# Kernel tuning notes

Measured on AMD Instinct MI355X. Metric: run time of the kernel, lower is better.

## Reference

```python
import jax, jax.numpy as jnp
import numpy as np

T, B, I, H = 512, 64, 256, 256
ACT_EXP2 = 7   # activation scale = 2^-7
W_EXP2 = 8     # weight scale = 2^-8
QMIN, QMAX = -128.0, 127.0  # int8 symmetric, zp=0


def fq(x, exp2_inv):
    """Fake-quantize (round/clamp/dequant) with straight-through estimator."""
    scale = 2.0 ** (-exp2_inv)
    y = jnp.clip(jnp.round(x / scale), QMIN, QMAX) * scale
    return x + jax.lax.stop_gradient(y - x)


def setup_inputs() -> dict:
    key = jax.random.key(0)
    k = jax.random.split(key, 5)
    x = jax.random.normal(k[0], (T, B, I), jnp.float32)
    h0 = jnp.zeros((B, H), jnp.float32)
    W = jax.random.normal(k[1], (I, 3 * H), jnp.float32) / np.sqrt(I)
    R = jax.random.normal(k[2], (H, 3 * H), jnp.float32) / np.sqrt(H)
    bx = jax.random.normal(k[3], (3 * H,), jnp.float32) * 0.1
    br = jax.random.normal(k[4], (3 * H,), jnp.float32) * 0.1
    return {"x": x, "h0": h0, "W": W, "R": R, "bx": bx, "br": br}


def gru_quant(x, h0, W, R, bx, br):
    # quantize weights/biases once (weight.W / weight.R / weight.bx / weight.br)
    Wq = fq(W, W_EXP2)
    Rq = fq(R, W_EXP2)
    bxq = fq(bx, W_EXP2)
    brq = fq(br, W_EXP2)
    # hoisted input matmul: Wx = fq(fq(x) @ Wq)  -> [T, B, 3H]
    Wx = fq(jnp.einsum('tbi,ij->tbj', fq(x, ACT_EXP2), Wq), ACT_EXP2)
    Hh = h0.shape[-1]
    bz, brg, bg = bxq[:Hh], bxq[Hh:2 * Hh], bxq[2 * Hh:]

    def step(h, wx_t):
        hq = fq(h, ACT_EXP2)                      # input.h
        Rh = fq(hq @ Rq, ACT_EXP2)                # matmul.Rh
        v = fq(Rh + brq, ACT_EXP2)                # op.Rh_add_br
        wz, wr, wg = wx_t[:, :Hh], wx_t[:, Hh:2 * Hh], wx_t[:, 2 * Hh:]
        vz, vr, vg = v[:, :Hh], v[:, Hh:2 * Hh], v[:, 2 * Hh:]
        z = fq(jax.nn.sigmoid(fq(wz + bz + vz, ACT_EXP2)), ACT_EXP2)  # gate.z
        r = fq(jax.nn.sigmoid(fq(wr + brg + vr, ACT_EXP2)), ACT_EXP2)  # gate.r
        rRh = fq(r * vg, ACT_EXP2)                # op.rRh
        g = fq(jnp.tanh(fq(wg + bg + rRh, ACT_EXP2)), ACT_EXP2)        # gate.g
        old = fq(z * h, ACT_EXP2)                 # op.old_contrib
        new = fq((1.0 - z) * g, ACT_EXP2)         # op.new_contrib
        h_new = old + new
        return h_new, h_new

    _, hs = jax.lax.scan(step, h0, Wx)  # hs: [T, B, H]
    return hs


def reference(x, h0, W, R, bx, br):
    return gru_quant(x, h0, W, R, bx, br)
```

## Files before the change

kernel.cpp:

```cpp
#include <hip/hip_runtime.h>
#include <hip/hip_bf16.h>
#include <stdint.h>


#define T_STEPS 512
#define BATCH   64
#define IDIM    256
#define HDIM    256
#define N3H     768

#if defined(__has_builtin)
#if __has_builtin(__builtin_amdgcn_sdot4)
#define DOT4(a,b,c) __builtin_amdgcn_sdot4((int)(a),(int)(b),(int)(c),false)
#endif
#endif
#ifndef DOT4
__device__ __forceinline__ int dot4_sw(uint32_t a, uint32_t b, int c){
  c += (int)(int8_t)(a)      * (int)(int8_t)(b);
  c += (int)(int8_t)(a>>8)   * (int)(int8_t)(b>>8);
  c += (int)(int8_t)(a>>16)  * (int)(int8_t)(b>>16);
  c += (int)(int8_t)(a>>24)  * (int)(int8_t)(b>>24);
  return c;
}
#define DOT4(a,b,c) dot4_sw((uint32_t)(a),(uint32_t)(b),(int)(c))
#endif

#define CHUNK(W,c) (((c)&3)==0 ? W[(c)>>2].x : ((c)&3)==1 ? W[(c)>>2].y : \
                    ((c)&3)==2 ? W[(c)>>2].z : W[(c)>>2].w)

__device__ __forceinline__ void barrier_lds() {
  asm volatile("s_waitcnt lgkmcnt(0)\n\ts_barrier" ::: "memory");
}

__device__ __forceinline__ int clamp8(int x)   { return min(127, max(-128, x)); }
__device__ __forceinline__ int rne_half(int y) { int t = y >> 1; return t + (t & y & 1); }
__device__ __forceinline__ int rne_s8(int s)   { return (s + 127 + ((s >> 8) & 1)) >> 8; }
__device__ __forceinline__ int rne_s7(int p)   { return (p + 63 + ((p >> 7) & 1)) >> 7; }

__device__ __forceinline__ int rneclamp(float v) {
  int q = (int)rintf(v);
  return min(127, max(-128, q));
}

__device__ __forceinline__ uint32_t packq4(float4 f, float sc) {
  uint32_t b0 = (uint32_t)(uint8_t)(int8_t)rneclamp(f.x * sc);
  uint32_t b1 = (uint32_t)(uint8_t)(int8_t)rneclamp(f.y * sc);
  uint32_t b2 = (uint32_t)(uint8_t)(int8_t)rneclamp(f.z * sc);
  uint32_t b3 = (uint32_t)(uint8_t)(int8_t)rneclamp(f.w * sc);
  return b0 | (b1 << 8) | (b2 << 16) | (b3 << 24);
}

__global__ void prep_kernel(const float* __restrict__ W, const float* __restrict__ R,
                            const float* __restrict__ bx, const float* __restrict__ br,
                            int8_t* __restrict__ Wq, int8_t* __restrict__ Rq,
                            int8_t* __restrict__ bx8, int8_t* __restrict__ br8) {
  const int NW = IDIM * N3H;
  int idx = blockIdx.x * 256 + threadIdx.x;
  if (idx < NW) {
    int k = idx / N3H, j = idx % N3H;
    Wq[((size_t)(k >> 4) * N3H + j) * 16 + (k & 15)] = (int8_t)rneclamp(W[idx] * 256.0f);
  } else if (idx < 2 * NW) {
    int i2 = idx - NW;
    int k = i2 / N3H, j = i2 % N3H;
    Rq[(size_t)j * HDIM + k] = (int8_t)rneclamp(R[i2] * 256.0f);
  } else if (idx < 2 * NW + N3H) {
    int i2 = idx - 2 * NW;
    bx8[i2] = (int8_t)rneclamp(bx[i2] * 256.0f);
  } else if (idx < 2 * NW + 2 * N3H) {
    int i2 = idx - 2 * NW - N3H;
    br8[i2] = (int8_t)rneclamp(br[i2] * 256.0f);
  }
}

__global__ __launch_bounds__(768, 1) void gemm_wx_kernel(
    const float* __restrict__ x, const int8_t* __restrict__ Wq,
    int8_t* __restrict__ WxQ8) {
  const int t = blockIdx.x;
  const int j = threadIdx.x;

  __shared__ uint4 xq4[64 * 16];
  uint32_t* xq = (uint32_t*)xq4;

  uint4 w[16];
  const uint4* wp = (const uint4*)Wq;
  #pragma unroll
  for (int kk = 0; kk < 16; ++kk) w[kk] = wp[kk * N3H + j];

  const float4* xg = (const float4*)(x) + (size_t)t * 4096;
  for (int i = j; i < 4096; i += 768) {
    float4 f = xg[i];
    xq[i] = packq4(f, 128.0f);
  }
  __syncthreads();

  for (int r = 0; r < 64; ++r) {
    int s = 0;
    #pragma unroll
    for (int kk = 0; kk < 16; ++kk) {
      uint4 hv = xq4[r * 16 + kk];
      s = DOT4(hv.x, w[kk].x, s);
      s = DOT4(hv.y, w[kk].y, s);
      s = DOT4(hv.z, w[kk].z, s);
      s = DOT4(hv.w, w[kk].w, s);
    }
    int q = clamp8(rne_s8(s));
    WxQ8[((size_t)r * T_STEPS + t) * N3H + j] = (int8_t)q;
  }
}

__global__ __launch_bounds__(256, 1) __attribute__((amdgpu_waves_per_eu(1, 1)))
void gru_rec6_kernel(
    const float* __restrict__ h0, const int8_t* __restrict__ Rq,
    const int8_t* __restrict__ bx8, const int8_t* __restrict__ br8,
    const int8_t* __restrict__ WxQ8, float* __restrict__ out) {
  const int b = blockIdx.x;
  const int j = threadIdx.x;
  const int lane = j & 63;

  __shared__ uint32_t hq[2][64];
  __shared__ int8_t lutS[256];
  __shared__ int8_t lutT[256];

  uint4 wz[16], wr[16], wg[16];
  {
    const uint4* pz = (const uint4*)(Rq + (size_t)j * HDIM);
    const uint4* pr = (const uint4*)(Rq + (size_t)(j + 256) * HDIM);
    const uint4* pg = (const uint4*)(Rq + (size_t)(j + 512) * HDIM);
    #pragma unroll
    for (int kk = 0; kk < 16; ++kk) { wz[kk] = pz[kk]; wr[kk] = pr[kk]; wg[kk] = pg[kk]; }
  }
  const int bz  = (int)bx8[j];
  const int brg = (int)bx8[j + 256];
  const int bg  = (int)bx8[j + 512];
  const int vbz = (int)br8[j];
  const int vbr = (int)br8[j + 256];
  const int vbg = (int)br8[j + 512];

  {
    double a = ((double)j - 128.0) / 128.0;
    lutS[j] = (int8_t)min(127, max(-128, (int)rint(128.0 / (1.0 + exp(-a)))));
    lutT[j] = (int8_t)min(127, max(-128, (int)rint(128.0 * tanh(a))));
  }
  int hi = (int)rintf(h0[b * HDIM + j] * 128.0f);
  ((int8_t*)&hq[0][0])[j] = (int8_t)clamp8(hi);
  __syncthreads();

  const int8_t* wxp = WxQ8 + (size_t)b * T_STEPS * N3H + j;
  float* outp = out + (size_t)b * HDIM + j;

  int wxA0 = (int)wxp[0],   wxA1 = (int)wxp[256],       wxA2 = (int)wxp[512];
  int wxB0 = (int)wxp[N3H], wxB1 = (int)wxp[N3H + 256], wxB2 = (int)wxp[N3H + 512];

  for (int t = 0; t < T_STEPS; ++t) {
    const int cur = t & 1, nxt = cur ^ 1;

    const int8_t* p = wxp + (size_t)min(t + 2, T_STEPS - 1) * N3H;
    int nz = (int)p[0], nr = (int)p[256], ng = (int)p[512];

    uint32_t hw = hq[cur][lane];
    int sz = 0, sr = 0, sg = 0;
    #pragma unroll
    for (int c = 0; c < 64; ++c) {
      int hc = __builtin_amdgcn_readlane((int)hw, c);
      sz = DOT4(hc, CHUNK(wz, c), sz);
      sr = DOT4(hc, CHUNK(wr, c), sr);
      sg = DOT4(hc, CHUNK(wg, c), sg);
    }
    int vz = clamp8(rne_half(2 * clamp8(rne_s8(sz)) + vbz));
    int vr = clamp8(rne_half(2 * clamp8(rne_s8(sr)) + vbr));
    int vg = clamp8(rne_half(2 * clamp8(rne_s8(sg)) + vbg));

    int az = clamp8(rne_half(2 * (wxA0 + vz) + bz));
    int zi = (int)lutS[az + 128];
    int ar = clamp8(rne_half(2 * (wxA1 + vr) + brg));
    int ri = (int)lutS[ar + 128];
    int rrh = clamp8(rne_s7(ri * vg));
    int ag = clamp8(rne_half(2 * (wxA2 + rrh) + bg));
    int gi = (int)lutT[ag + 128];
    int oldi = clamp8(rne_s7(zi * hi));
    int newi = clamp8(rne_s7((128 - zi) * gi));
    hi = oldi + newi;
    outp[(size_t)t * BATCH * HDIM] = (float)hi * (1.0f / 128.0f);
    ((int8_t*)&hq[nxt][0])[j] = (int8_t)clamp8(hi);

    wxA0 = wxB0; wxA1 = wxB1; wxA2 = wxB2;
    wxB0 = nz;   wxB1 = nr;   wxB2 = ng;

    barrier_lds();
  }
}

extern "C" void kernel_launch(void* const* d_in, const int* in_sizes, int n_in,
                              void* d_out, int out_size, void* d_ws, size_t ws_size,
                              hipStream_t stream) {
  const float* x  = (const float*)d_in[0];
  const float* h0 = (const float*)d_in[1];
  const float* W  = (const float*)d_in[2];
  const float* R  = (const float*)d_in[3];
  const float* bx = (const float*)d_in[4];
  const float* br = (const float*)d_in[5];
  float* out = (float*)d_out;

  const size_t NW = (size_t)IDIM * N3H;
  int8_t* Wq  = (int8_t*)d_ws;
  int8_t* Rq  = Wq + NW;
  int8_t* bx8 = Rq + NW;
  int8_t* br8 = bx8 + N3H;
  int8_t* WxQ8 = br8 + N3H;

  {
    int total = (int)(2 * NW + 2 * N3H);
    int blocks = (total + 255) / 256;
    prep_kernel<<<blocks, 256, 0, stream>>>(W, R, bx, br, Wq, Rq, bx8, br8);
  }
  gemm_wx_kernel<<<T_STEPS, 768, 0, stream>>>(x, Wq, WxQ8);
  gru_rec6_kernel<<<BATCH, 256, 0, stream>>>(h0, Rq, bx8, br8, WxQ8, out);
}
```

Baseline: 473.9 us.

## Split recurrent matvec across 768 threads, one gate column per thread

The recurrent kernel now launches 768 threads per batch block instead of 256. Each thread computes one of the 3H gate outputs, holding a single 256-byte weight column in registers rather than three, and the R weights are stored in the same k-chunked layout as W. Gate pre-activations go through a shared-memory buffer plus an extra barrier per step, and the first 256 threads then do the elementwise GRU update. This spreads the serial per-step dot-product work over three times as many waves, at the cost of a second barrier each step and idle threads during the elementwise phase.

```diff
diff --git a/kernel.cpp b/kernel.cpp
--- a/kernel.cpp
+++ b/kernel.cpp
@@ -62,7 +62,7 @@
   } else if (idx < 2 * NW) {
     int i2 = idx - NW;
     int k = i2 / N3H, j = i2 % N3H;
-    Rq[(size_t)j * HDIM + k] = (int8_t)rneclamp(R[i2] * 256.0f);
+    Rq[((size_t)(k >> 4) * N3H + j) * 16 + (k & 15)] = (int8_t)rneclamp(R[i2] * 256.0f);
   } else if (idx < 2 * NW + N3H) {
     int i2 = idx - 2 * NW;
     bx8[i2] = (int8_t)rneclamp(bx[i2] * 256.0f);
@@ -108,8 +108,8 @@
   }
 }
 
-__global__ __launch_bounds__(256, 1) __attribute__((amdgpu_waves_per_eu(1, 1)))
-void gru_rec6_kernel(
+__global__ __launch_bounds__(768, 3)
+void gru_rec13_kernel(
     const float* __restrict__ h0, const int8_t* __restrict__ Rq,
     const int8_t* __restrict__ bx8, const int8_t* __restrict__ br8,
     const int8_t* __restrict__ WxQ8, float* __restrict__ out) {
@@ -118,74 +118,81 @@
   const int lane = j & 63;
 
   __shared__ uint32_t hq[2][64];
+  __shared__ int8_t vbuf[N3H];
   __shared__ int8_t lutS[256];
   __shared__ int8_t lutT[256];
 
-  uint4 wz[16], wr[16], wg[16];
+  uint4 w[16];
   {
-    const uint4* pz = (const uint4*)(Rq + (size_t)j * HDIM);
-    const uint4* pr = (const uint4*)(Rq + (size_t)(j + 256) * HDIM);
-    const uint4* pg = (const uint4*)(Rq + (size_t)(j + 512) * HDIM);
-    #pragma unroll
-    for (int kk = 0; kk < 16; ++kk) { wz[kk] = pz[kk]; wr[kk] = pr[kk]; wg[kk] = pg[kk]; }
-  }
-  const int bz  = (int)bx8[j];
-  const int brg = (int)bx8[j + 256];
-  const int bg  = (int)bx8[j + 512];
-  const int vbz = (int)br8[j];
-  const int vbr = (int)br8[j + 256];
-  const int vbg = (int)br8[j + 512];
-
-  {
+    const uint4* rp = (const uint4*)Rq;
+    #pragma unroll
+    for (int kk = 0; kk < 16; ++kk) w[kk] = rp[kk * N3H + j];
+  }
+  const int vb = (int)br8[j];
+
+  int hi = 0, bzc = 0, brc = 0, bgc = 0;
+  const int8_t* wxp = WxQ8 + (size_t)b * T_STEPS * N3H + j;
+  int wxA0 = 0, wxA1 = 0, wxA2 = 0, wxB0 = 0, wxB1 = 0, wxB2 = 0;
+  if (j < 256) {
     double a = ((double)j - 128.0) / 128.0;
     lutS[j] = (int8_t)min(127, max(-128, (int)rint(128.0 / (1.0 + exp(-a)))));
     lutT[j] = (int8_t)min(127, max(-128, (int)rint(128.0 * tanh(a))));
-  }
-  int hi = (int)rintf(h0[b * HDIM + j] * 128.0f);
-  ((int8_t*)&hq[0][0])[j] = (int8_t)clamp8(hi);
+    bzc = (int)bx8[j];
+    brc = (int)bx8[j + 256];
+    bgc = (int)bx8[j + 512];
+    hi = (int)rintf(h0[b * HDIM + j] * 128.0f);
+    ((int8_t*)&hq[0][0])[j] = (int8_t)clamp8(hi);
+    wxA0 = (int)wxp[0];   wxA1 = (int)wxp[256];       wxA2 = (int)wxp[512];
+    wxB0 = (int)wxp[N3H]; wxB1 = (int)wxp[N3H + 256]; wxB2 = (int)wxp[N3H + 512];
+  }
   __syncthreads();
 
-  const int8_t* wxp = WxQ8 + (size_t)b * T_STEPS * N3H + j;
-  float* outp = out + (size_t)b * HDIM + j;
-
-  int wxA0 = (int)wxp[0],   wxA1 = (int)wxp[256],       wxA2 = (int)wxp[512];
-  int wxB0 = (int)wxp[N3H], wxB1 = (int)wxp[N3H + 256], wxB2 = (int)wxp[N3H + 512];
+  float* outp = out + (size_t)b * HDIM + (j < 256 ? j : 0);
 
   for (int t = 0; t < T_STEPS; ++t) {
     const int cur = t & 1, nxt = cur ^ 1;
 
-    const int8_t* p = wxp + (size_t)min(t + 2, T_STEPS - 1) * N3H;
-    int nz = (int)p[0], nr = (int)p[256], ng = (int)p[512];
+    #pragma unroll
+    for (int kk = 0; kk < 16; ++kk)
+      asm volatile("" : "+v"(w[kk].x), "+v"(w[kk].y), "+v"(w[kk].z), "+v"(w[kk].w));
+
+    int nz = 0, nr = 0, ng = 0;
+    if (j < 256) {
+      const int8_t* p = wxp + (size_t)min(t + 2, T_STEPS - 1) * N3H;
+      nz = (int)p[0]; nr = (int)p[256]; ng = (int)p[512];
+    }
 
     uint32_t hw = hq[cur][lane];
-    int sz = 0, sr = 0, sg = 0;
-    #pragma unroll
-    for (int c = 0; c < 64; ++c) {
-      int hc = __builtin_amdgcn_readlane((int)hw, c);
-      sz = DOT4(hc, CHUNK(wz, c), sz);
-      sr = DOT4(hc, CHUNK(wr, c), sr);
-      sg = DOT4(hc, CHUNK(wg, c), sg);
-    }
-    int vz = clamp8(rne_half(2 * clamp8(rne_s8(sz)) + vbz));
-    int vr = clamp8(rne_half(2 * clamp8(rne_s8(sr)) + vbr));
-    int vg = clamp8(rne_half(2 * clamp8(rne_s8(sg)) + vbg));
-
-    int az = clamp8(rne_half(2 * (wxA0 + vz) + bz));
-    int zi = (int)lutS[az + 128];
-    int ar = clamp8(rne_half(2 * (wxA1 + vr) + brg));
-    int ri = (int)lutS[ar + 128];
-    int rrh = clamp8(rne_s7(ri * vg));
-    int ag = clamp8(rne_half(2 * (wxA2 + rrh) + bg));
-    int gi = (int)lutT[ag + 128];
-    int oldi = clamp8(rne_s7(zi * hi));
-    int newi = clamp8(rne_s7((128 - zi) * gi));
-    hi = oldi + newi;
-    outp[(size_t)t * BATCH * HDIM] = (float)hi * (1.0f / 128.0f);
-    ((int8_t*)&hq[nxt][0])[j] = (int8_t)clamp8(hi);
-
-    wxA0 = wxB0; wxA1 = wxB1; wxA2 = wxB2;
-    wxB0 = nz;   wxB1 = nr;   wxB2 = ng;
-
+    int s0 = 0, s1 = 0;
+    #pragma unroll
+    for (int c = 0; c < 64; c += 2) {
+      int h0c = __builtin_amdgcn_readlane((int)hw, c);
+      int h1c = __builtin_amdgcn_readlane((int)hw, c + 1);
+      s0 = DOT4(h0c, CHUNK(w, c), s0);
+      s1 = DOT4(h1c, CHUNK(w, c + 1), s1);
+    }
+    int s = s0 + s1;
+    int v = clamp8(rne_half(2 * clamp8(rne_s8(s)) + vb));
+    vbuf[j] = (int8_t)v;
+    barrier_lds();
+
+    if (j < 256) {
+      int vz = (int)vbuf[j], vr = (int)vbuf[j + 256], vg = (int)vbuf[j + 512];
+      int az = clamp8(rne_half(2 * (wxA0 + vz) + bzc));
+      int zi = (int)lutS[az + 128];
+      int ar = clamp8(rne_half(2 * (wxA1 + vr) + brc));
+      int ri = (int)lutS[ar + 128];
+      int rrh = clamp8(rne_s7(ri * vg));
+      int ag = clamp8(rne_half(2 * (wxA2 + rrh) + bgc));
+      int gi = (int)lutT[ag + 128];
+      int oldi = clamp8(rne_s7(zi * hi));
+      int newi = clamp8(rne_s7((128 - zi) * gi));
+      hi = oldi + newi;
+      outp[(size_t)t * BATCH * HDIM] = (float)hi * (1.0f / 128.0f);
+      ((int8_t*)&hq[nxt][0])[j] = (int8_t)clamp8(hi);
+      wxA0 = wxB0; wxA1 = wxB1; wxA2 = wxB2;
+      wxB0 = nz;   wxB1 = nr;   wxB2 = ng;
+    }
     barrier_lds();
   }
 }
@@ -214,5 +221,5 @@
     prep_kernel<<<blocks, 256, 0, stream>>>(W, R, bx, br, Wq, Rq, bx8, br8);
   }
   gemm_wx_kernel<<<T_STEPS, 768, 0, stream>>>(x, Wq, WxQ8);
-  gru_rec6_kernel<<<BATCH, 256, 0, stream>>>(h0, Rq, bx8, br8, WxQ8, out);
-}
+  gru_rec13_kernel<<<BATCH, 768, 0, stream>>>(h0, Rq, bx8, br8, WxQ8, out);
+}
```

Result: slower. 629.0 us (+32.7%).

## Split recurrent K dimension across two thread halves and pair two batches per block

Applied to the files above, without the earlier changes.

The recurrent kernel now runs 512 threads per block, each handling two batch rows. Each half of the block computes half of the K reduction for both batches, swaps partial sums through LDS, and then finishes one batch's gate math. The aim is to halve the serial dot-product chain per timestep and reuse register-resident weights across two batches. In exchange it adds a second barrier per step, extra LDS traffic, and uses only 32 blocks.

```diff
diff --git a/kernel.cpp b/kernel.cpp
--- a/kernel.cpp
+++ b/kernel.cpp
@@ -108,48 +108,57 @@
   }
 }
 
-__global__ __launch_bounds__(256, 1) __attribute__((amdgpu_waves_per_eu(1, 1)))
-void gru_rec6_kernel(
+__global__ __launch_bounds__(512, 1)
+void gru_rec17_kernel(
     const float* __restrict__ h0, const int8_t* __restrict__ Rq,
     const int8_t* __restrict__ bx8, const int8_t* __restrict__ br8,
     const int8_t* __restrict__ WxQ8, float* __restrict__ out) {
-  const int b = blockIdx.x;
-  const int j = threadIdx.x;
-  const int lane = j & 63;
-
-  __shared__ uint32_t hq[2][64];
+  const int bA = blockIdx.x * 2;
+  const int bB = bA + 1;
+  const int tid = threadIdx.x;
+  const int kh  = tid >> 8;
+  const int j   = tid & 255;
+  const int lane = tid & 63;
+
+  __shared__ uint32_t hqA[2][64];
+  __shared__ uint32_t hqB[2][64];
+  __shared__ int pubA[3][256];
+  __shared__ int pubB[3][256];
   __shared__ int8_t lutS[256];
   __shared__ int8_t lutT[256];
 
-  uint4 wz[16], wr[16], wg[16];
+  uint4 wz[8], wr[8], wg[8];
   {
-    const uint4* pz = (const uint4*)(Rq + (size_t)j * HDIM);
-    const uint4* pr = (const uint4*)(Rq + (size_t)(j + 256) * HDIM);
-    const uint4* pg = (const uint4*)(Rq + (size_t)(j + 512) * HDIM);
+    const uint4* pz = (const uint4*)(Rq + (size_t)j * HDIM)         + kh * 8;
+    const uint4* pr = (const uint4*)(Rq + (size_t)(j + 256) * HDIM) + kh * 8;
+    const uint4* pg = (const uint4*)(Rq + (size_t)(j + 512) * HDIM) + kh * 8;
     #pragma unroll
-    for (int kk = 0; kk < 16; ++kk) { wz[kk] = pz[kk]; wr[kk] = pr[kk]; wg[kk] = pg[kk]; }
-  }
-  const int bz  = (int)bx8[j];
-  const int brg = (int)bx8[j + 256];
-  const int bg  = (int)bx8[j + 512];
+    for (int kk = 0; kk < 8; ++kk) { wz[kk] = pz[kk]; wr[kk] = pr[kk]; wg[kk] = pg[kk]; }
+  }
+  const int myb = kh ? bB : bA;
+  const int bzc = (int)bx8[j];
+  const int brc = (int)bx8[j + 256];
+  const int bgc = (int)bx8[j + 512];
   const int vbz = (int)br8[j];
   const int vbr = (int)br8[j + 256];
   const int vbg = (int)br8[j + 512];
 
-  {
+  if (tid < 256) {
     double a = ((double)j - 128.0) / 128.0;
     lutS[j] = (int8_t)min(127, max(-128, (int)rint(128.0 / (1.0 + exp(-a)))));
     lutT[j] = (int8_t)min(127, max(-128, (int)rint(128.0 * tanh(a))));
-  }
-  int hi = (int)rintf(h0[b * HDIM + j] * 128.0f);
-  ((int8_t*)&hq[0][0])[j] = (int8_t)clamp8(hi);
-  __syncthreads();
-
-  const int8_t* wxp = WxQ8 + (size_t)b * T_STEPS * N3H + j;
-  float* outp = out + (size_t)b * HDIM + j;
-
+    int hA0 = (int)rintf(h0[bA * HDIM + j] * 128.0f);
+    int hB0 = (int)rintf(h0[bB * HDIM + j] * 128.0f);
+    ((int8_t*)&hqA[0][0])[j] = (int8_t)clamp8(hA0);
+    ((int8_t*)&hqB[0][0])[j] = (int8_t)clamp8(hB0);
+  }
+  int hi = (int)rintf(h0[myb * HDIM + j] * 128.0f);
+
+  const int8_t* wxp = WxQ8 + (size_t)myb * T_STEPS * N3H + j;
+  float* outp = out + (size_t)myb * HDIM + j;
   int wxA0 = (int)wxp[0],   wxA1 = (int)wxp[256],       wxA2 = (int)wxp[512];
   int wxB0 = (int)wxp[N3H], wxB1 = (int)wxp[N3H + 256], wxB2 = (int)wxp[N3H + 512];
+  __syncthreads();
 
   for (int t = 0; t < T_STEPS; ++t) {
     const int cur = t & 1, nxt = cur ^ 1;
@@ -157,35 +166,47 @@
     const int8_t* p = wxp + (size_t)min(t + 2, T_STEPS - 1) * N3H;
     int nz = (int)p[0], nr = (int)p[256], ng = (int)p[512];
 
-    uint32_t hw = hq[cur][lane];
-    int sz = 0, sr = 0, sg = 0;
+    uint32_t hwA = hqA[cur][kh * 32 + (lane & 31)];
+    uint32_t hwB = hqB[cur][kh * 32 + (lane & 31)];
+    int szA = 0, srA = 0, sgA = 0, szB = 0, srB = 0, sgB = 0;
     #pragma unroll
-    for (int c = 0; c < 64; ++c) {
-      int hc = __builtin_amdgcn_readlane((int)hw, c);
-      sz = DOT4(hc, CHUNK(wz, c), sz);
-      sr = DOT4(hc, CHUNK(wr, c), sr);
-      sg = DOT4(hc, CHUNK(wg, c), sg);
+    for (int c = 0; c < 32; ++c) {
+      int ha = __builtin_amdgcn_readlane((int)hwA, c);
+      int hb = __builtin_amdgcn_readlane((int)hwB, c);
+      szA = DOT4(ha, CHUNK(wz, c), szA);
+      szB = DOT4(hb, CHUNK(wz, c), szB);
+      srA = DOT4(ha, CHUNK(wr, c), srA);
+      srB = DOT4(hb, CHUNK(wr, c), srB);
+      sgA = DOT4(ha, CHUNK(wg, c), sgA);
+      sgB = DOT4(hb, CHUNK(wg, c), sgB);
     }
-    int vz = clamp8(rne_half(2 * clamp8(rne_s8(sz)) + vbz));
-    int vr = clamp8(rne_half(2 * clamp8(rne_s8(sr)) + vbr));
-    int vg = clamp8(rne_half(2 * clamp8(rne_s8(sg)) + vbg));
-
-    int az = clamp8(rne_half(2 * (wxA0 + vz) + bz));
-    int zi = (int)lutS[az + 128];
-    int ar = clamp8(rne_half(2 * (wxA1 + vr) + brg));
-    int ri = (int)lutS[ar + 128];
-    int rrh = clamp8(rne_s7(ri * vg));
-    int ag = clamp8(rne_half(2 * (wxA2 + rrh) + bg));
-    int gi = (int)lutT[ag + 128];
-    int oldi = clamp8(rne_s7(zi * hi));
-    int newi = clamp8(rne_s7((128 - zi) * gi));
-    hi = oldi + newi;
-    outp[(size_t)t * BATCH * HDIM] = (float)hi * (1.0f / 128.0f);
-    ((int8_t*)&hq[nxt][0])[j] = (int8_t)clamp8(hi);
-
-    wxA0 = wxB0; wxA1 = wxB1; wxA2 = wxB2;
-    wxB0 = nz;   wxB1 = nr;   wxB2 = ng;
-
+    if (kh) { pubA[0][j] = szA; pubA[1][j] = srA; pubA[2][j] = sgA; }
+    else    { pubB[0][j] = szB; pubB[1][j] = srB; pubB[2][j] = sgB; }
+    barrier_lds();
+
+    {
+      int sz, sr, sg;
+      if (kh == 0) { sz = szA + pubA[0][j]; sr = srA + pubA[1][j]; sg = sgA + pubA[2][j]; }
+      else         { sz = szB + pubB[0][j]; sr = srB + pubB[1][j]; sg = sgB + pubB[2][j]; }
+      int vz = clamp8(rne_half(2 * clamp8(rne_s8(sz)) + vbz));
+      int vr = clamp8(rne_half(2 * clamp8(rne_s8(sr)) + vbr));
+      int vg = clamp8(rne_half(2 * clamp8(rne_s8(sg)) + vbg));
+      int az = clamp8(rne_half(2 * (wxA0 + vz) + bzc));
+      int zi = (int)lutS[az + 128];
+      int ar = clamp8(rne_half(2 * (wxA1 + vr) + brc));
+      int ri = (int)lutS[ar + 128];
+      int rrh = clamp8(rne_s7(ri * vg));
+      int ag = clamp8(rne_half(2 * (wxA2 + rrh) + bgc));
+      int gi = (int)lutT[ag + 128];
+      int oldi = clamp8(rne_s7(zi * hi));
+      int newi = clamp8(rne_s7((128 - zi) * gi));
+      hi = oldi + newi;
+      outp[(size_t)t * BATCH * HDIM] = (float)hi * (1.0f / 128.0f);
+      if (kh == 0) ((int8_t*)&hqA[nxt][0])[j] = (int8_t)clamp8(hi);
+      else         ((int8_t*)&hqB[nxt][0])[j] = (int8_t)clamp8(hi);
+      wxA0 = wxB0; wxA1 = wxB1; wxA2 = wxB2;
+      wxB0 = nz;   wxB1 = nr;   wxB2 = ng;
+    }
     barrier_lds();
   }
 }
@@ -214,5 +235,5 @@
     prep_kernel<<<blocks, 256, 0, stream>>>(W, R, bx, br, Wq, Rq, bx8, br8);
   }
   gemm_wx_kernel<<<T_STEPS, 768, 0, stream>>>(x, Wq, WxQ8);
-  gru_rec6_kernel<<<BATCH, 256, 0, stream>>>(h0, Rq, bx8, br8, WxQ8, out);
-}
+  gru_rec17_kernel<<<BATCH / 2, 512, 0, stream>>>(h0, Rq, bx8, br8, WxQ8, out);
+}
```

After: 858.3 us. 1.81x slower.
